# Kernel optimization log

Measured on AMD Instinct MI355X. Metric: run time of the kernel, lower is better.

Reference implementation:

```python
import jax, jax.numpy as jnp
import numpy as np
from jax import lax

BITWIDTH = 7
EPS = 1e-5


def ti_quant(x):
    """TiFloatToInt8: per-tensor int8 quantization with power-of-2 scale."""
    rng = jnp.max(jnp.abs(x))
    bw = jnp.ceil(jnp.log2(rng))
    exp = bw - BITWIDTH
    q = jnp.clip(jnp.round(x * 2.0 ** (BITWIDTH - bw)), -128.0, 127.0)
    return q, exp


def ti_conv(xv, xe, wv, we, pad):
    """TiConv2d: integer conv (simulated in f32, all values int-valued),
    int32 accumulate, then shift back to 8 bits; exponents add."""
    acc = lax.conv_general_dilated(
        xv, wv, window_strides=(1, 1), padding=[(pad, pad), (pad, pad)],
        dimension_numbers=("NCHW", "OIHW", "NCHW"))
    rng = jnp.max(jnp.abs(acc))
    bw = jnp.ceil(jnp.log2(rng))
    shift = jnp.maximum(bw - BITWIDTH, 0.0)
    q = jnp.clip(jnp.round(acc * 2.0 ** (-shift)), -128.0, 127.0)
    return q, xe + we + shift


def batchnorm(x, gamma, beta):
    # training-mode BN: batch statistics over (N, H, W)
    mean = jnp.mean(x, axis=(0, 2, 3), keepdims=True)
    var = jnp.var(x, axis=(0, 2, 3), keepdims=True)
    g = gamma[None, :, None, None]
    b = beta[None, :, None, None]
    return g * (x - mean) * lax.rsqrt(var + EPS) + b


def setup_inputs() -> dict:
    key = jax.random.key(0)
    k0, k1, k2, k3, k4 = jax.random.split(key, 5)
    B, Cin, Cout, H, W = 32, 128, 256, 56, 56
    x_val = jax.random.randint(k0, (B, Cin, H, W), -128, 128, dtype=jnp.int32)
    x_exp = jnp.zeros((), jnp.float32) - 7.0
    wDW = jnp.round(jnp.clip(jax.random.normal(k1, (Cin, Cin, 3, 3), jnp.float32) * 32.0, -128.0, 127.0))
    wDW_exp = jnp.zeros((), jnp.float32) - 9.0
    wPW = jnp.round(jnp.clip(jax.random.normal(k2, (Cout, Cin, 1, 1), jnp.float32) * 32.0, -128.0, 127.0))
    wPW_exp = jnp.zeros((), jnp.float32) - 9.0
    gamma1 = jnp.ones((Cin,), jnp.float32) + 0.1 * jax.random.normal(k3, (Cin,), jnp.float32)
    beta1 = jnp.zeros((Cin,), jnp.float32)
    gamma2 = jnp.ones((Cout,), jnp.float32) + 0.1 * jax.random.normal(k4, (Cout,), jnp.float32)
    beta2 = jnp.zeros((Cout,), jnp.float32)
    return {"x_val": x_val, "x_exp": x_exp, "wDW": wDW, "wDW_exp": wDW_exp,
            "wPW": wPW, "wPW_exp": wPW_exp, "gamma1": gamma1, "beta1": beta1,
            "gamma2": gamma2, "beta2": beta2}


def reference(x_val, x_exp, wDW, wDW_exp, wPW, wPW_exp, gamma1, beta1, gamma2, beta2):
    xv = x_val.astype(jnp.float32)
    # convDW (3x3, in->in, pad=1)
    q, e = ti_conv(xv, x_exp, wDW, wDW_exp, 1)
    # dequant -> bn1 -> quant
    f = batchnorm(q * 2.0 ** e, gamma1, beta1)
    q, e = ti_quant(f)
    # TiReLU on int values
    q = jnp.maximum(q, 0.0)
    # convPW (1x1, in->out)
    q, e = ti_conv(q, e, wPW, wPW_exp, 0)
    # dequant -> bn2 -> quant -> relu
    f = batchnorm(q * 2.0 ** e, gamma2, beta2)
    q, e = ti_quant(f)
    q = jnp.maximum(q, 0.0)
    return q.astype(jnp.int8), e
```

## Files before the change

kernel.cpp:

```cpp
#include <hip/hip_runtime.h>
#include <cstdint>
#include <cstddef>

#define C1 128
#define C2 256
#define Hh 56
#define Wd 56
#define HW 3136
#define NHW 100352
#define N1 ((size_t)12845056)
#define N2 ((size_t)25690112)
#define XPSZ ((size_t)13778944)

typedef int v4i __attribute__((ext_vector_type(4)));
typedef int v16i __attribute__((ext_vector_type(16)));

static constexpr size_t OFF_XP = 0;
static constexpr size_t OFF_ACC1 = XPSZ;
static constexpr size_t OFF_Q1 = OFF_ACC1 + 4 * N1;
static constexpr size_t OFF_Q3 = OFF_Q1 + N1;
static constexpr size_t OFF_WQ1 = OFF_Q3 + N2;
static constexpr size_t OFF_WQ2 = OFF_WQ1 + 147456;
static constexpr size_t OFF_STATS = OFF_WQ2 + 32768;

struct Stats {
  int absmax1, absmax2, pad0, pad1;
  float scale1, e1, s2, e2;
  float scaleq2, e3, sf, ef;
  int sum1[C1]; unsigned sumsq1[C1];
  int min1[C1], max1[C1];
  float A1[C1], B1c[C1];
  int sum2[C2]; unsigned sumsq2[C2];
  int min2[C2], max2[C2];
  float A2[C2], B2c[C2];
};

__global__ void k_init(Stats* st) {
  int t = threadIdx.x;
  if (t == 0) { st->absmax1 = 0; st->absmax2 = 0; }
  for (int c = t; c < C1; c += 256) {
    st->sum1[c] = 0; st->sumsq1[c] = 0; st->min1[c] = 127; st->max1[c] = -128;
  }
  for (int c = t; c < C2; c += 256) {
    st->sum2[c] = 0; st->sumsq2[c] = 0; st->min2[c] = 127; st->max2[c] = -128;
  }
}

__global__ __launch_bounds__(256) void k_prep_x2(
    const int* __restrict__ x, signed char* __restrict__ xp) {
  __shared__ signed char lds[56 * 132];
  int t = threadIdx.x;
  int hh = blockIdx.x;
  int n = blockIdx.y;
  int* xpw = (int*)(xp + ((size_t)n * 58 + hh) * 7424);
  if (hh == 0 || hh == 57) {
    for (int o = t; o < 1856; o += 256) xpw[o] = 0;
    return;
  }
  int h = hh - 1;
  const int* xb = x + (size_t)n * C1 * HW + h * 56;
  for (int idx = t; idx < 7168; idx += 256) {
    int c = idx / 56, w = idx - c * 56;
    lds[w * 132 + c] = (signed char)xb[(size_t)c * HW + w];
  }
  __syncthreads();
  for (int o = t; o < 1856; o += 256) {
    int kb = o / 232, r = o - kb * 232, ww = r >> 2, cw = r & 3;
    int val = (ww == 0 || ww == 57) ? 0
              : *(const int*)&lds[(ww - 1) * 132 + kb * 16 + cw * 4];
    xpw[o] = val;
  }
}

__global__ void k_prep_w1(const float* __restrict__ wDW, signed char* __restrict__ wq1t) {
  int idx = blockIdx.x * 256 + threadIdx.x;
  if (idx >= 128 * 1152) return;
  int co = idx / 1152, r = idx - co * 1152;
  int ci = r / 9, pos = r - ci * 9;
  int k = pos * 128 + ci;
  wq1t[(size_t)(k >> 4) * 2048 + co * 16 + (k & 15)] = (signed char)(int)wDW[idx];
}

__global__ void k_prep_w2(const float* __restrict__ wPW, signed char* __restrict__ wq2t) {
  int i = blockIdx.x * 256 + threadIdx.x;
  int co = i >> 7, ci = i & 127;
  wq2t[(size_t)(ci >> 4) * 4096 + co * 16 + (ci & 15)] = (signed char)(int)wPW[i];
}

__device__ inline v4i ld16_lds(const signed char* p) {
  const int2* q = (const int2*)p;
  int2 lo = q[0], hi = q[1];
  v4i r; r[0] = lo.x; r[1] = lo.y; r[2] = hi.x; r[3] = hi.y;
  return r;
}

__global__ __launch_bounds__(256, 2) void k_conv1s(
    const signed char* __restrict__ xp, const signed char* __restrict__ wq1t,
    int* __restrict__ acc1, Stats* st) {
  __shared__ int reda[4];
  int t = threadIdx.x, lane = t & 63, wave = t >> 6;
  int half = lane >> 5, l31 = lane & 31;
  size_t g0 = (size_t)blockIdx.x * 256;

  const signed char* ab[2];
#pragma unroll
  for (int i = 0; i < 2; ++i) {
    size_t gm = g0 + wave * 64 + i * 32 + l31;
    int n = (int)(gm / HW);
    int p = (int)(gm - (size_t)n * HW);
    int h = p / 56, w = p - h * 56;
    ab[i] = xp + ((size_t)n * 58 + h) * 7424 + w * 16 + half * 928;
  }
  const signed char* bb[4];
#pragma unroll
  for (int j = 0; j < 4; ++j)
    bb[j] = wq1t + (size_t)(j * 32 + l31) * 16 + half * 2048;

  v16i a1[2][4];
#pragma unroll
  for (int i = 0; i < 2; ++i)
#pragma unroll
    for (int j = 0; j < 4; ++j)
#pragma unroll
      for (int r = 0; r < 16; ++r) a1[i][j][r] = 0;

#pragma unroll
  for (int pos = 0; pos < 9; ++pos) {
    int kh = pos / 3, kw = pos - kh * 3;
    const signed char* a0p = ab[0] + kh * 7424 + kw * 16;
    const signed char* a1p = ab[1] + kh * 7424 + kw * 16;
#pragma unroll
    for (int kb = 0; kb < 8; kb += 2) {
      v4i af0 = *(const v4i*)(a0p + kb * 928);
      v4i af1 = *(const v4i*)(a1p + kb * 928);
      v4i bf[4];
#pragma unroll
      for (int j = 0; j < 4; ++j)
        bf[j] = *(const v4i*)(bb[j] + pos * 16384 + kb * 2048);
#pragma unroll
      for (int j = 0; j < 4; ++j) {
        a1[0][j] = __builtin_amdgcn_mfma_i32_32x32x32_i8(af0, bf[j], a1[0][j], 0, 0, 0);
        a1[1][j] = __builtin_amdgcn_mfma_i32_32x32x32_i8(af1, bf[j], a1[1][j], 0, 0, 0);
      }
    }
  }

  int am = 0;
#pragma unroll
  for (int i = 0; i < 2; ++i)
#pragma unroll
    for (int j = 0; j < 4; ++j)
#pragma unroll
      for (int r = 0; r < 16; ++r) am = max(am, abs(a1[i][j][r]));
  for (int off = 32; off; off >>= 1) am = max(am, __shfl_down(am, off, 64));
  if (lane == 0) reda[wave] = am;
  __syncthreads();
  if (t == 0)
    atomicMax(&st->absmax1, max(max(reda[0], reda[1]), max(reda[2], reda[3])));

  int* ob = acc1 + (size_t)blockIdx.x * 32768;
#pragma unroll
  for (int i = 0; i < 2; ++i)
#pragma unroll
    for (int j = 0; j < 4; ++j)
#pragma unroll
      for (int reg = 0; reg < 16; ++reg)
        ob[(((wave * 2 + i) * 4 + j) * 16 + reg) * 64 + lane] = a1[i][j][reg];
}

__global__ __launch_bounds__(256, 2) void k_qstats1(
    const int* __restrict__ acc1, signed char* __restrict__ q1, Stats* st,
    const float* __restrict__ x_exp, const float* __restrict__ wDW_exp) {
  __shared__ int qti[256 * 34];
  __shared__ int psum[C1], psq[C1], pmn[C1], pmx[C1];
  signed char* qt = (signed char*)qti;
  int t = threadIdx.x, lane = t & 63, wave = t >> 6;
  int half = lane >> 5, l31 = lane & 31;

  if (t < C1) { psum[t] = 0; psq[t] = 0; pmn[t] = 127; pmx[t] = -128; }
  __syncthreads();

  int v1 = st->absmax1;
  int pw = 31 - __clz(v1 | 1);
  int bw = ((v1 & (v1 - 1)) == 0) ? pw : pw + 1;
  int sh = max(bw - 7, 0);
  float scale1 = exp2f((float)(-sh));
  if (blockIdx.x == 0 && t == 0)
    st->e1 = x_exp[0] + wDW_exp[0] + (float)sh;

  const int* ib = acc1 + (size_t)blockIdx.x * 32768;
#pragma unroll
  for (int j = 0; j < 4; ++j) {
    int sj = 0, sqj = 0, mnj = 127, mxj = -128;
    int c = j * 32 + l31;
#pragma unroll
    for (int i = 0; i < 2; ++i)
#pragma unroll
      for (int reg = 0; reg < 16; ++reg) {
        int av = ib[(((wave * 2 + i) * 4 + j) * 16 + reg) * 64 + lane];
        int row = (reg & 3) + 8 * (reg >> 2) + 4 * half;
        int pix = wave * 64 + i * 32 + row;
        float r = rintf((float)av * scale1);
        r = fminf(fmaxf(r, -128.f), 127.f);
        int qi = (int)r;
        qt[pix * 136 + c] = (signed char)qi;
        sj += qi; sqj += qi * qi; mnj = min(mnj, qi); mxj = max(mxj, qi);
      }
    sj += __shfl_down(sj, 32, 64);
    sqj += __shfl_down(sqj, 32, 64);
    mnj = min(mnj, __shfl_down(mnj, 32, 64));
    mxj = max(mxj, __shfl_down(mxj, 32, 64));
    if (half == 0) {
      atomicAdd(&psum[c], sj); atomicAdd(&psq[c], sqj);
      atomicMin(&pmn[c], mnj); atomicMax(&pmx[c], mxj);
    }
  }
  __syncthreads();
  if (t < C1) {
    atomicAdd(&st->sum1[t], psum[t]);
    atomicAdd(&st->sumsq1[t], (unsigned)psq[t]);
    atomicMin(&st->min1[t], pmn[t]);
    atomicMax(&st->max1[t], pmx[t]);
  }
  int* q1w = (int*)(q1 + (size_t)blockIdx.x * 256 * 128);
  for (int idx = t; idx < 8192; idx += 256) {
    int pix = idx >> 5, c4 = idx & 31;
    q1w[idx] = qti[pix * 34 + c4];
  }
}

template <int STORE>
__global__ __launch_bounds__(256, 2) void k_conv2t(
    const signed char* __restrict__ q1, const signed char* __restrict__ wq2t,
    signed char* __restrict__ q3, Stats* st, const float* __restrict__ wPW_exp) {
  __shared__ int qti[128 * 34];
  __shared__ signed char stg[128 * 264];
  __shared__ int psum[C2], psq[C2], pmn[C2], pmx[C2];
  __shared__ int reda[4];
  signed char* qt = (signed char*)qti;

  int t = threadIdx.x, lane = t & 63, wave = t >> 6;
  int half = lane >> 5, l31 = lane & 31;
  size_t g0 = (size_t)blockIdx.x * 128;

  if (STORE) { psum[t] = 0; psq[t] = 0; pmn[t] = 127; pmx[t] = -128; }

  int c4 = t & 31;
  float Av[4], Bv[4];
#pragma unroll
  for (int jj = 0; jj < 4; ++jj) {
    Av[jj] = st->A1[c4 * 4 + jj];
    Bv[jj] = st->B1c[c4 * 4 + jj];
  }
  float s2 = st->s2;
  const int* q1w = (const int*)(q1 + g0 * 128);
#pragma unroll
  for (int k = 0; k < 16; ++k) {
    int idx = k * 256 + t;
    int v = q1w[idx];
    int pix = idx >> 5;
    int outv = 0;
#pragma unroll
    for (int jj = 0; jj < 4; ++jj) {
      int b = (signed char)(v >> (8 * jj));
      float y = Av[jj] * (float)b + Bv[jj];
      float r = rintf(y * s2);
      r = fminf(fmaxf(r, -128.f), 127.f);
      r = fmaxf(r, 0.f);
      outv |= ((int)r & 0xff) << (8 * jj);
    }
    qti[pix * 34 + c4] = outv;
  }
  __syncthreads();

  v16i acc[8];
#pragma unroll
  for (int j = 0; j < 8; ++j)
#pragma unroll
    for (int r = 0; r < 16; ++r) acc[j][r] = 0;

#pragma unroll
  for (int ks = 0; ks < 4; ++ks) {
    v4i af = ld16_lds(&qt[(wave * 32 + l31) * 136 + half * 16 + ks * 32]);
#pragma unroll
    for (int j = 0; j < 8; ++j) {
      v4i bf = *(const v4i*)(wq2t + (size_t)(ks * 2 + half) * 4096 + (j * 32 + l31) * 16);
      acc[j] = __builtin_amdgcn_mfma_i32_32x32x32_i8(af, bf, acc[j], 0, 0, 0);
    }
  }

  if (STORE == 0) {
    int am2 = 0;
#pragma unroll
    for (int j = 0; j < 8; ++j)
#pragma unroll
      for (int r = 0; r < 16; ++r) am2 = max(am2, abs(acc[j][r]));
    for (int off = 32; off; off >>= 1) am2 = max(am2, __shfl_down(am2, off, 64));
    if (lane == 0) reda[wave] = am2;
    __syncthreads();
    if (t == 0)
      atomicMax(&st->absmax2, max(max(reda[0], reda[1]), max(reda[2], reda[3])));
  } else {
    int v2 = st->absmax2;
    int pw = 31 - __clz(v2 | 1);
    int bw = ((v2 & (v2 - 1)) == 0) ? pw : pw + 1;
    int sh2 = max(bw - 7, 0);
    float scale2 = exp2f((float)(-sh2));
    if (blockIdx.x == 0 && t == 0)
      st->e3 = st->e2 + wPW_exp[0] + (float)sh2;
#pragma unroll
    for (int j = 0; j < 8; ++j) {
      int c = j * 32 + l31;
      int sj = 0, sqj = 0, mnj = 127, mxj = -128;
#pragma unroll
      for (int reg = 0; reg < 16; ++reg) {
        int row = (reg & 3) + 8 * (reg >> 2) + 4 * half;
        float r = rintf((float)acc[j][reg] * scale2);
        r = fminf(fmaxf(r, -128.f), 127.f);
        int qi = (int)r;
        stg[(wave * 32 + row) * 264 + c] = (signed char)qi;
        sj += qi; sqj += qi * qi; mnj = min(mnj, qi); mxj = max(mxj, qi);
      }
      sj += __shfl_down(sj, 32, 64);
      sqj += __shfl_down(sqj, 32, 64);
      mnj = min(mnj, __shfl_down(mnj, 32, 64));
      mxj = max(mxj, __shfl_down(mxj, 32, 64));
      if (half == 0) {
        atomicAdd(&psum[c], sj); atomicAdd(&psq[c], sqj);
        atomicMin(&pmn[c], mnj); atomicMax(&pmx[c], mxj);
      }
    }
    __syncthreads();
    atomicAdd(&st->sum2[t], psum[t]);
    atomicAdd(&st->sumsq2[t], (unsigned)psq[t]);
    atomicMin(&st->min2[t], pmn[t]);
    atomicMax(&st->max2[t], pmx[t]);
    int* q3w = (int*)(q3 + g0 * 256);
#pragma unroll
    for (int k = 0; k < 32; ++k) {
      int idx = k * 256 + t;
      int pix = idx >> 6, cw = idx & 63;
      q3w[idx] = *(const int*)&stg[pix * 264 + cw * 4];
    }
  }
}

__global__ void k_bn(const int* __restrict__ sums,
                     const unsigned* __restrict__ sumsqs,
                     const int* __restrict__ mins, const int* __restrict__ maxs,
                     const float* __restrict__ gamma, const float* __restrict__ beta,
                     const float* __restrict__ e_in,
                     float* A, float* Bc, float* s_out, float* e_out,
                     float* e_extra, int C) {
  __shared__ float red[4];
  int t = threadIdx.x;
  float e1 = *e_in;
  double meanq = (double)sums[t] / (double)NHW;
  double varq = (double)sumsqs[t] / (double)NHW - meanq * meanq;
  float se = exp2f(e1);
  float mean = (float)meanq * se;
  float var = (float)varq * se * se;
  float rsq = 1.0f / sqrtf(var + 1e-5f);
  float g = gamma[t], b = beta[t];
  float Avv = g * se * rsq;
  float Bvv = b - g * mean * rsq;
  A[t] = Avv; Bc[t] = Bvv;
  float cand = fmaxf(fabsf(Avv * (float)mins[t] + Bvv), fabsf(Avv * (float)maxs[t] + Bvv));
  for (int off = 32; off; off >>= 1) cand = fmaxf(cand, __shfl_down(cand, off, 64));
  int wave = t >> 6, lane = t & 63;
  if (lane == 0) red[wave] = cand;
  __syncthreads();
  if (t == 0) {
    float rng = red[0];
    for (int i = 1; i < C / 64; i++) rng = fmaxf(rng, red[i]);
    float bwv = ceilf(log2f(rng));
    *s_out = exp2f(7.0f - bwv);
    *e_out = bwv - 7.0f;
    if (e_extra) *e_extra = bwv - 7.0f;
  }
}

__global__ __launch_bounds__(256) void k_out(
    const signed char* __restrict__ q3, const Stats* __restrict__ st,
    float* __restrict__ out) {
  __shared__ signed char lds[64 * 260];
  int t = threadIdx.x, lane = t & 63, wave = t >> 6;
  size_t g0 = (size_t)blockIdx.x * 64;
  int n = (int)(g0 / HW), p0 = (int)(g0 - (size_t)n * HW);
  const int* q3w = (const int*)(q3 + g0 * 256);
#pragma unroll
  for (int k = 0; k < 16; ++k) {
    int idx = k * 256 + t;
    int pix = idx >> 6, cw = idx & 63;
    *(int*)&lds[pix * 260 + cw * 4] = q3w[idx];
  }
  __syncthreads();
  float sf = st->sf;
  float* ob = out + (size_t)n * C2 * HW + p0 + lane;
#pragma unroll
  for (int cg = 0; cg < 16; ++cg) {
    int v = *(const int*)&lds[lane * 260 + wave * 64 + cg * 4];
#pragma unroll
    for (int jj = 0; jj < 4; ++jj) {
      int c = wave * 64 + cg * 4 + jj;
      float y = st->A2[c] * (float)((signed char)(v >> (8 * jj))) + st->B2c[c];
      float r = rintf(y * sf);
      r = fminf(fmaxf(r, -128.f), 127.f);
      ob[(size_t)c * HW] = fmaxf(r, 0.f);
    }
  }
}

extern "C" void kernel_launch(void* const* d_in, const int* in_sizes, int n_in,
                              void* d_out, int out_size, void* d_ws, size_t ws_size,
                              hipStream_t stream) {
  const int* x = (const int*)d_in[0];
  const float* x_exp = (const float*)d_in[1];
  const float* wDW = (const float*)d_in[2];
  const float* wDW_exp = (const float*)d_in[3];
  const float* wPW = (const float*)d_in[4];
  const float* wPW_exp = (const float*)d_in[5];
  const float* gamma1 = (const float*)d_in[6];
  const float* beta1 = (const float*)d_in[7];
  const float* gamma2 = (const float*)d_in[8];
  const float* beta2 = (const float*)d_in[9];
  float* out = (float*)d_out;

  char* ws = (char*)d_ws;
  signed char* xp2 = (signed char*)(ws + OFF_XP);
  int* acc1 = (int*)(ws + OFF_ACC1);
  signed char* q1 = (signed char*)(ws + OFF_Q1);
  signed char* q3 = (signed char*)(ws + OFF_Q3);
  signed char* wq1t = (signed char*)(ws + OFF_WQ1);
  signed char* wq2t = (signed char*)(ws + OFF_WQ2);
  Stats* st = (Stats*)(ws + OFF_STATS);

  hipLaunchKernelGGL(k_init, dim3(1), dim3(256), 0, stream, st);
  hipLaunchKernelGGL(k_prep_x2, dim3(58, 32), dim3(256), 0, stream, x, xp2);
  hipLaunchKernelGGL(k_prep_w1, dim3(576), dim3(256), 0, stream, wDW, wq1t);
  hipLaunchKernelGGL(k_prep_w2, dim3(128), dim3(256), 0, stream, wPW, wq2t);

  hipLaunchKernelGGL(k_conv1s, dim3(392), dim3(256), 0, stream,
                     xp2, wq1t, acc1, st);
  hipLaunchKernelGGL(k_qstats1, dim3(392), dim3(256), 0, stream,
                     acc1, q1, st, x_exp, wDW_exp);
  hipLaunchKernelGGL(k_bn, dim3(1), dim3(C1), 0, stream,
                     st->sum1, st->sumsq1, st->min1, st->max1, gamma1, beta1,
                     &st->e1, st->A1, st->B1c, &st->s2, &st->e2, (float*)nullptr, C1);

  hipLaunchKernelGGL(k_conv2t<0>, dim3(784), dim3(256), 0, stream,
                     q1, wq2t, q3, st, wPW_exp);
  hipLaunchKernelGGL(k_conv2t<1>, dim3(784), dim3(256), 0, stream,
                     q1, wq2t, q3, st, wPW_exp);
  hipLaunchKernelGGL(k_bn, dim3(1), dim3(C2), 0, stream,
                     st->sum2, st->sumsq2, st->min2, st->max2, gamma2, beta2,
                     &st->e3, st->A2, st->B2c, &st->sf, &st->ef, out + N2, C2);
  hipLaunchKernelGGL(k_out, dim3(1568), dim3(256), 0, stream, q3, st, out);
}
```

Before: 295.8 us.

## Fuse conv1 with quant and BN1 via cooperative grid sync; recompute conv2 instead of storing q3

Merges the four prep kernels into one launch. Replaces the conv1 plus quant-stats plus BN1 chain with a single cooperative kernel that keeps accumulators in registers across grid syncs, so the int32 acc1 tensor never goes to memory. The q3 intermediate is dropped: a third conv2 pass recomputes the 1x1 conv and writes the final output directly, with BN2 coefficients computed per block. This trades extra MFMA work and redundant per-block BN math for less HBM traffic and fewer launches, and relies on all 392 blocks being co-resident, with a fallback path if the cooperative launch fails.

```diff
diff --git a/kernel.cpp b/kernel.cpp
--- a/kernel.cpp
+++ b/kernel.cpp
@@ -1,6 +1,9 @@
 #include <hip/hip_runtime.h>
+#include <hip/hip_cooperative_groups.h>
 #include <cstdint>
 #include <cstddef>
+
+namespace cg = cooperative_groups;
 
 #define C1 128
 #define C2 256
@@ -18,25 +21,63 @@
 static constexpr size_t OFF_XP = 0;
 static constexpr size_t OFF_ACC1 = XPSZ;
 static constexpr size_t OFF_Q1 = OFF_ACC1 + 4 * N1;
-static constexpr size_t OFF_Q3 = OFF_Q1 + N1;
-static constexpr size_t OFF_WQ1 = OFF_Q3 + N2;
+static constexpr size_t OFF_WQ1 = OFF_Q1 + N1;
 static constexpr size_t OFF_WQ2 = OFF_WQ1 + 147456;
 static constexpr size_t OFF_STATS = OFF_WQ2 + 32768;
 
 struct Stats {
   int absmax1, absmax2, pad0, pad1;
-  float scale1, e1, s2, e2;
-  float scaleq2, e3, sf, ef;
+  float e1, e2, e3, s2v;
+  float A1[C1], B1c[C1];
   int sum1[C1]; unsigned sumsq1[C1];
   int min1[C1], max1[C1];
-  float A1[C1], B1c[C1];
   int sum2[C2]; unsigned sumsq2[C2];
   int min2[C2], max2[C2];
-  float A2[C2], B2c[C2];
 };
 
-__global__ void k_init(Stats* st) {
-  int t = threadIdx.x;
+__global__ __launch_bounds__(256) void k_pre(
+    const int* __restrict__ x, signed char* __restrict__ xp,
+    const float* __restrict__ wDW, signed char* __restrict__ wq1t,
+    const float* __restrict__ wPW, signed char* __restrict__ wq2t,
+    Stats* st) {
+  __shared__ signed char lds[56 * 132];
+  int t = threadIdx.x, bid = blockIdx.x;
+  if (bid < 1856) {
+    int hh = bid % 58, n = bid / 58;
+    int* xpw = (int*)(xp + ((size_t)n * 58 + hh) * 7424);
+    if (hh == 0 || hh == 57) {
+      for (int o = t; o < 1856; o += 256) xpw[o] = 0;
+      return;
+    }
+    int h = hh - 1;
+    const int* xb = x + (size_t)n * C1 * HW + h * 56;
+    for (int idx = t; idx < 7168; idx += 256) {
+      int c = idx / 56, w = idx - c * 56;
+      lds[w * 132 + c] = (signed char)xb[(size_t)c * HW + w];
+    }
+    __syncthreads();
+    for (int o = t; o < 1856; o += 256) {
+      int kb = o / 232, r = o - kb * 232, ww = r >> 2, cw = r & 3;
+      int val = (ww == 0 || ww == 57) ? 0
+                : *(const int*)&lds[(ww - 1) * 132 + kb * 16 + cw * 4];
+      xpw[o] = val;
+    }
+    return;
+  }
+  if (bid < 2432) {
+    int idx = (bid - 1856) * 256 + t;
+    int co = idx / 1152, r = idx - co * 1152;
+    int ci = r / 9, pos = r - ci * 9;
+    int k = pos * 128 + ci;
+    wq1t[(size_t)(k >> 4) * 2048 + co * 16 + (k & 15)] = (signed char)(int)wDW[idx];
+    return;
+  }
+  if (bid < 2560) {
+    int i = (bid - 2432) * 256 + t;
+    int co = i >> 7, ci = i & 127;
+    wq2t[(size_t)(ci >> 4) * 4096 + co * 16 + (ci & 15)] = (signed char)(int)wPW[i];
+    return;
+  }
   if (t == 0) { st->absmax1 = 0; st->absmax2 = 0; }
   for (int c = t; c < C1; c += 256) {
     st->sum1[c] = 0; st->sumsq1[c] = 0; st->min1[c] = 127; st->max1[c] = -128;
@@ -44,47 +85,6 @@
   for (int c = t; c < C2; c += 256) {
     st->sum2[c] = 0; st->sumsq2[c] = 0; st->min2[c] = 127; st->max2[c] = -128;
   }
-}
-
-__global__ __launch_bounds__(256) void k_prep_x2(
-    const int* __restrict__ x, signed char* __restrict__ xp) {
-  __shared__ signed char lds[56 * 132];
-  int t = threadIdx.x;
-  int hh = blockIdx.x;
-  int n = blockIdx.y;
-  int* xpw = (int*)(xp + ((size_t)n * 58 + hh) * 7424);
-  if (hh == 0 || hh == 57) {
-    for (int o = t; o < 1856; o += 256) xpw[o] = 0;
-    return;
-  }
-  int h = hh - 1;
-  const int* xb = x + (size_t)n * C1 * HW + h * 56;
-  for (int idx = t; idx < 7168; idx += 256) {
-    int c = idx / 56, w = idx - c * 56;
-    lds[w * 132 + c] = (signed char)xb[(size_t)c * HW + w];
-  }
-  __syncthreads();
-  for (int o = t; o < 1856; o += 256) {
-    int kb = o / 232, r = o - kb * 232, ww = r >> 2, cw = r & 3;
-    int val = (ww == 0 || ww == 57) ? 0
-              : *(const int*)&lds[(ww - 1) * 132 + kb * 16 + cw * 4];
-    xpw[o] = val;
-  }
-}
-
-__global__ void k_prep_w1(const float* __restrict__ wDW, signed char* __restrict__ wq1t) {
-  int idx = blockIdx.x * 256 + threadIdx.x;
-  if (idx >= 128 * 1152) return;
-  int co = idx / 1152, r = idx - co * 1152;
-  int ci = r / 9, pos = r - ci * 9;
-  int k = pos * 128 + ci;
-  wq1t[(size_t)(k >> 4) * 2048 + co * 16 + (k & 15)] = (signed char)(int)wDW[idx];
-}
-
-__global__ void k_prep_w2(const float* __restrict__ wPW, signed char* __restrict__ wq2t) {
-  int i = blockIdx.x * 256 + threadIdx.x;
-  int co = i >> 7, ci = i & 127;
-  wq2t[(size_t)(ci >> 4) * 4096 + co * 16 + (ci & 15)] = (signed char)(int)wPW[i];
 }
 
 __device__ inline v4i ld16_lds(const signed char* p) {
@@ -92,6 +92,165 @@
   int2 lo = q[0], hi = q[1];
   v4i r; r[0] = lo.x; r[1] = lo.y; r[2] = hi.x; r[3] = hi.y;
   return r;
+}
+
+__device__ inline float bn_affine_v(int sum, unsigned sumsq, int mn, int mx,
+                                    float g, float b, float e_in,
+                                    float* Aout, float* Bout) {
+  double meanq = (double)sum / (double)NHW;
+  double varq = (double)sumsq / (double)NHW - meanq * meanq;
+  float se = exp2f(e_in);
+  float mean = (float)meanq * se;
+  float var = (float)varq * se * se;
+  float rsq = 1.0f / sqrtf(var + 1e-5f);
+  float Avv = g * se * rsq;
+  float Bvv = b - g * mean * rsq;
+  *Aout = Avv; *Bout = Bvv;
+  return fmaxf(fabsf(Avv * (float)mn + Bvv), fabsf(Avv * (float)mx + Bvv));
+}
+
+__global__ __launch_bounds__(256, 2) void k_conv1f(
+    const signed char* __restrict__ xp, const signed char* __restrict__ wq1t,
+    signed char* __restrict__ q1, Stats* st,
+    const float* __restrict__ x_exp, const float* __restrict__ wDW_exp,
+    const float* __restrict__ gamma1, const float* __restrict__ beta1) {
+  __shared__ int reda[4];
+  __shared__ int vbro;
+  __shared__ int qti[256 * 34];
+  __shared__ int psum[C1], psq[C1], pmn[C1], pmx[C1];
+  __shared__ float redc[2];
+  signed char* qt = (signed char*)qti;
+  int t = threadIdx.x, lane = t & 63, wave = t >> 6;
+  int half = lane >> 5, l31 = lane & 31;
+  size_t g0 = (size_t)blockIdx.x * 256;
+
+  const signed char* ab[2];
+#pragma unroll
+  for (int i = 0; i < 2; ++i) {
+    size_t gm = g0 + wave * 64 + i * 32 + l31;
+    int n = (int)(gm / HW);
+    int p = (int)(gm - (size_t)n * HW);
+    int h = p / 56, w = p - h * 56;
+    ab[i] = xp + ((size_t)n * 58 + h) * 7424 + w * 16 + half * 928;
+  }
+  const signed char* bb[4];
+#pragma unroll
+  for (int j = 0; j < 4; ++j)
+    bb[j] = wq1t + (size_t)(j * 32 + l31) * 16 + half * 2048;
+
+  v16i a1[2][4];
+#pragma unroll
+  for (int i = 0; i < 2; ++i)
+#pragma unroll
+    for (int j = 0; j < 4; ++j)
+#pragma unroll
+      for (int r = 0; r < 16; ++r) a1[i][j][r] = 0;
+
+#pragma unroll
+  for (int pos = 0; pos < 9; ++pos) {
+    int kh = pos / 3, kw = pos - kh * 3;
+    const signed char* a0p = ab[0] + kh * 7424 + kw * 16;
+    const signed char* a1p = ab[1] + kh * 7424 + kw * 16;
+#pragma unroll
+    for (int kb = 0; kb < 8; kb += 2) {
+      v4i af0 = *(const v4i*)(a0p + kb * 928);
+      v4i af1 = *(const v4i*)(a1p + kb * 928);
+      v4i bf[4];
+#pragma unroll
+      for (int j = 0; j < 4; ++j)
+        bf[j] = *(const v4i*)(bb[j] + pos * 16384 + kb * 2048);
+#pragma unroll
+      for (int j = 0; j < 4; ++j) {
+        a1[0][j] = __builtin_amdgcn_mfma_i32_32x32x32_i8(af0, bf[j], a1[0][j], 0, 0, 0);
+        a1[1][j] = __builtin_amdgcn_mfma_i32_32x32x32_i8(af1, bf[j], a1[1][j], 0, 0, 0);
+      }
+    }
+  }
+
+  int am = 0;
+#pragma unroll
+  for (int i = 0; i < 2; ++i)
+#pragma unroll
+    for (int j = 0; j < 4; ++j)
+#pragma unroll
+      for (int r = 0; r < 16; ++r) am = max(am, abs(a1[i][j][r]));
+  for (int off = 32; off; off >>= 1) am = max(am, __shfl_down(am, off, 64));
+  if (lane == 0) reda[wave] = am;
+  __syncthreads();
+  if (t == 0)
+    atomicMax(&st->absmax1, max(max(reda[0], reda[1]), max(reda[2], reda[3])));
+  if (t < C1) { psum[t] = 0; psq[t] = 0; pmn[t] = 127; pmx[t] = -128; }
+
+  cg::this_grid().sync();
+
+  if (t == 0) vbro = atomicMax(&st->absmax1, 0);
+  __syncthreads();
+  int v1 = vbro;
+  int pw = 31 - __clz(v1 | 1);
+  int bw = ((v1 & (v1 - 1)) == 0) ? pw : pw + 1;
+  int sh = max(bw - 7, 0);
+  float scale1 = exp2f((float)(-sh));
+  if (blockIdx.x == 0 && t == 0)
+    st->e1 = x_exp[0] + wDW_exp[0] + (float)sh;
+
+#pragma unroll
+  for (int j = 0; j < 4; ++j) {
+    int sj = 0, sqj = 0, mnj = 127, mxj = -128;
+    int c = j * 32 + l31;
+#pragma unroll
+    for (int i = 0; i < 2; ++i)
+#pragma unroll
+      for (int reg = 0; reg < 16; ++reg) {
+        int av = a1[i][j][reg];
+        int row = (reg & 3) + 8 * (reg >> 2) + 4 * half;
+        int pix = wave * 64 + i * 32 + row;
+        float r = rintf((float)av * scale1);
+        r = fminf(fmaxf(r, -128.f), 127.f);
+        int qi = (int)r;
+        qt[pix * 136 + c] = (signed char)qi;
+        sj += qi; sqj += qi * qi; mnj = min(mnj, qi); mxj = max(mxj, qi);
+      }
+    sj += __shfl_down(sj, 32, 64);
+    sqj += __shfl_down(sqj, 32, 64);
+    mnj = min(mnj, __shfl_down(mnj, 32, 64));
+    mxj = max(mxj, __shfl_down(mxj, 32, 64));
+    if (half == 0) {
+      atomicAdd(&psum[c], sj); atomicAdd(&psq[c], sqj);
+      atomicMin(&pmn[c], mnj); atomicMax(&pmx[c], mxj);
+    }
+  }
+  __syncthreads();
+  if (t < C1) {
+    atomicAdd(&st->sum1[t], psum[t]);
+    atomicAdd(&st->sumsq1[t], (unsigned)psq[t]);
+    atomicMin(&st->min1[t], pmn[t]);
+    atomicMax(&st->max1[t], pmx[t]);
+  }
+  int* q1w = (int*)(q1 + g0 * 128);
+  for (int idx = t; idx < 8192; idx += 256)
+    q1w[idx] = qti[(idx >> 5) * 34 + (idx & 31)];
+
+  cg::this_grid().sync();
+
+  if (blockIdx.x == 0) {
+    if (t < C1) {
+      int sm = atomicAdd(&st->sum1[t], 0);
+      unsigned sq = atomicAdd(&st->sumsq1[t], 0u);
+      int mn = atomicMin(&st->min1[t], 127);
+      int mx = atomicMax(&st->max1[t], -128);
+      float cand = bn_affine_v(sm, sq, mn, mx, gamma1[t], beta1[t], st->e1,
+                               &st->A1[t], &st->B1c[t]);
+      for (int off = 32; off; off >>= 1) cand = fmaxf(cand, __shfl_down(cand, off, 64));
+      if ((t & 63) == 0) redc[t >> 6] = cand;
+    }
+    __syncthreads();
+    if (t == 0) {
+      float rng = fmaxf(redc[0], redc[1]);
+      float bwv = ceilf(log2f(rng));
+      st->s2v = exp2f(7.0f - bwv);
+      st->e2 = bwv - 7.0f;
+    }
+  }
 }
 
 __global__ __launch_bounds__(256, 2) void k_conv1s(
@@ -223,18 +382,33 @@
     atomicMax(&st->max1[t], pmx[t]);
   }
   int* q1w = (int*)(q1 + (size_t)blockIdx.x * 256 * 128);
-  for (int idx = t; idx < 8192; idx += 256) {
-    int pix = idx >> 5, c4 = idx & 31;
-    q1w[idx] = qti[pix * 34 + c4];
-  }
-}
-
-template <int STORE>
-__global__ __launch_bounds__(256, 2) void k_conv2t(
+  for (int idx = t; idx < 8192; idx += 256)
+    q1w[idx] = qti[(idx >> 5) * 34 + (idx & 31)];
+}
+
+__global__ void k_bn1f(Stats* st, const float* __restrict__ gamma1,
+                       const float* __restrict__ beta1) {
+  __shared__ float red[2];
+  int t = threadIdx.x;
+  float cand = bn_affine_v(st->sum1[t], st->sumsq1[t], st->min1[t], st->max1[t],
+                           gamma1[t], beta1[t], st->e1, &st->A1[t], &st->B1c[t]);
+  for (int off = 32; off; off >>= 1) cand = fmaxf(cand, __shfl_down(cand, off, 64));
+  if ((t & 63) == 0) red[t >> 6] = cand;
+  __syncthreads();
+  if (t == 0) {
+    float rng = fmaxf(red[0], red[1]);
+    float bwv = ceilf(log2f(rng));
+    st->s2v = exp2f(7.0f - bwv);
+    st->e2 = bwv - 7.0f;
+  }
+}
+
+template <int PASS>
+__global__ __launch_bounds__(256, 2) void k_conv2(
     const signed char* __restrict__ q1, const signed char* __restrict__ wq2t,
-    signed char* __restrict__ q3, Stats* st, const float* __restrict__ wPW_exp) {
+    Stats* st, const float* __restrict__ wPW_exp) {
   __shared__ int qti[128 * 34];
-  __shared__ signed char stg[128 * 264];
+  __shared__ float A1l[C1], B1l[C1];
   __shared__ int psum[C2], psq[C2], pmn[C2], pmx[C2];
   __shared__ int reda[4];
   signed char* qt = (signed char*)qti;
@@ -243,16 +417,18 @@
   int half = lane >> 5, l31 = lane & 31;
   size_t g0 = (size_t)blockIdx.x * 128;
 
-  if (STORE) { psum[t] = 0; psq[t] = 0; pmn[t] = 127; pmx[t] = -128; }
+  if (t < C1) { A1l[t] = st->A1[t]; B1l[t] = st->B1c[t]; }
+  if (PASS) { psum[t] = 0; psq[t] = 0; pmn[t] = 127; pmx[t] = -128; }
+  __syncthreads();
+  float s2 = st->s2v;
 
   int c4 = t & 31;
   float Av[4], Bv[4];
 #pragma unroll
   for (int jj = 0; jj < 4; ++jj) {
-    Av[jj] = st->A1[c4 * 4 + jj];
-    Bv[jj] = st->B1c[c4 * 4 + jj];
-  }
-  float s2 = st->s2;
+    Av[jj] = A1l[c4 * 4 + jj];
+    Bv[jj] = B1l[c4 * 4 + jj];
+  }
   const int* q1w = (const int*)(q1 + g0 * 128);
 #pragma unroll
   for (int k = 0; k < 16; ++k) {
@@ -263,7 +439,7 @@
 #pragma unroll
     for (int jj = 0; jj < 4; ++jj) {
       int b = (signed char)(v >> (8 * jj));
-      float y = Av[jj] * (float)b + Bv[jj];
+      float y = __builtin_fmaf(Av[jj], (float)b, Bv[jj]);
       float r = rintf(y * s2);
       r = fminf(fmaxf(r, -128.f), 127.f);
       r = fmaxf(r, 0.f);
@@ -289,7 +465,7 @@
     }
   }
 
-  if (STORE == 0) {
+  if (PASS == 0) {
     int am2 = 0;
 #pragma unroll
     for (int j = 0; j < 8; ++j)
@@ -314,11 +490,9 @@
       int sj = 0, sqj = 0, mnj = 127, mxj = -128;
 #pragma unroll
       for (int reg = 0; reg < 16; ++reg) {
-        int row = (reg & 3) + 8 * (reg >> 2) + 4 * half;
         float r = rintf((float)acc[j][reg] * scale2);
         r = fminf(fmaxf(r, -128.f), 127.f);
         int qi = (int)r;
-        stg[(wave * 32 + row) * 264 + c] = (signed char)qi;
         sj += qi; sqj += qi * qi; mnj = min(mnj, qi); mxj = max(mxj, qi);
       }
       sj += __shfl_down(sj, 32, 64);
@@ -335,78 +509,117 @@
     atomicAdd(&st->sumsq2[t], (unsigned)psq[t]);
     atomicMin(&st->min2[t], pmn[t]);
     atomicMax(&st->max2[t], pmx[t]);
-    int* q3w = (int*)(q3 + g0 * 256);
-#pragma unroll
-    for (int k = 0; k < 32; ++k) {
-      int idx = k * 256 + t;
-      int pix = idx >> 6, cw = idx & 63;
-      q3w[idx] = *(const int*)&stg[pix * 264 + cw * 4];
-    }
-  }
-}
-
-__global__ void k_bn(const int* __restrict__ sums,
-                     const unsigned* __restrict__ sumsqs,
-                     const int* __restrict__ mins, const int* __restrict__ maxs,
-                     const float* __restrict__ gamma, const float* __restrict__ beta,
-                     const float* __restrict__ e_in,
-                     float* A, float* Bc, float* s_out, float* e_out,
-                     float* e_extra, int C) {
-  __shared__ float red[4];
-  int t = threadIdx.x;
-  float e1 = *e_in;
-  double meanq = (double)sums[t] / (double)NHW;
-  double varq = (double)sumsqs[t] / (double)NHW - meanq * meanq;
-  float se = exp2f(e1);
-  float mean = (float)meanq * se;
-  float var = (float)varq * se * se;
-  float rsq = 1.0f / sqrtf(var + 1e-5f);
-  float g = gamma[t], b = beta[t];
-  float Avv = g * se * rsq;
-  float Bvv = b - g * mean * rsq;
-  A[t] = Avv; Bc[t] = Bvv;
-  float cand = fmaxf(fabsf(Avv * (float)mins[t] + Bvv), fabsf(Avv * (float)maxs[t] + Bvv));
-  for (int off = 32; off; off >>= 1) cand = fmaxf(cand, __shfl_down(cand, off, 64));
-  int wave = t >> 6, lane = t & 63;
-  if (lane == 0) red[wave] = cand;
+  }
+}
+
+__global__ __launch_bounds__(256, 2) void k_out2(
+    const signed char* __restrict__ q1, const signed char* __restrict__ wq2t,
+    Stats* st, const float* __restrict__ gamma2, const float* __restrict__ beta2,
+    float* __restrict__ out) {
+  __shared__ int qti[128 * 34];
+  __shared__ __align__(16) signed char stg[128 * 264];
+  __shared__ float A1l[C1], B1l[C1], A2l[C2], B2l[C2];
+  __shared__ float red2[4], se2[2];
+  signed char* qt = (signed char*)qti;
+
+  int t = threadIdx.x, lane = t & 63, wave = t >> 6;
+  int half = lane >> 5, l31 = lane & 31;
+  size_t g0 = (size_t)blockIdx.x * 128;
+
+  if (t < C1) { A1l[t] = st->A1[t]; B1l[t] = st->B1c[t]; }
+  {
+    float cand = bn_affine_v(st->sum2[t], st->sumsq2[t], st->min2[t], st->max2[t],
+                             gamma2[t], beta2[t], st->e3, &A2l[t], &B2l[t]);
+    for (int off = 32; off; off >>= 1) cand = fmaxf(cand, __shfl_down(cand, off, 64));
+    if ((t & 63) == 0) red2[t >> 6] = cand;
+  }
   __syncthreads();
   if (t == 0) {
-    float rng = red[0];
-    for (int i = 1; i < C / 64; i++) rng = fmaxf(rng, red[i]);
+    float rng = fmaxf(fmaxf(red2[0], red2[1]), fmaxf(red2[2], red2[3]));
     float bwv = ceilf(log2f(rng));
-    *s_out = exp2f(7.0f - bwv);
-    *e_out = bwv - 7.0f;
-    if (e_extra) *e_extra = bwv - 7.0f;
-  }
-}
-
-__global__ __launch_bounds__(256) void k_out(
-    const signed char* __restrict__ q3, const Stats* __restrict__ st,
-    float* __restrict__ out) {
-  __shared__ signed char lds[64 * 260];
-  int t = threadIdx.x, lane = t & 63, wave = t >> 6;
-  size_t g0 = (size_t)blockIdx.x * 64;
-  int n = (int)(g0 / HW), p0 = (int)(g0 - (size_t)n * HW);
-  const int* q3w = (const int*)(q3 + g0 * 256);
+    se2[0] = exp2f(7.0f - bwv); se2[1] = bwv - 7.0f;
+  }
+  __syncthreads();
+  float s2 = st->s2v, sf = se2[0];
+  if (blockIdx.x == 0 && t == 0) out[N2] = se2[1];
+
+  int c4 = t & 31;
+  float Av[4], Bv[4];
+#pragma unroll
+  for (int jj = 0; jj < 4; ++jj) {
+    Av[jj] = A1l[c4 * 4 + jj];
+    Bv[jj] = B1l[c4 * 4 + jj];
+  }
+  const int* q1w = (const int*)(q1 + g0 * 128);
 #pragma unroll
   for (int k = 0; k < 16; ++k) {
     int idx = k * 256 + t;
-    int pix = idx >> 6, cw = idx & 63;
-    *(int*)&lds[pix * 260 + cw * 4] = q3w[idx];
-  }
-  __syncthreads();
-  float sf = st->sf;
-  float* ob = out + (size_t)n * C2 * HW + p0 + lane;
-#pragma unroll
-  for (int cg = 0; cg < 16; ++cg) {
-    int v = *(const int*)&lds[lane * 260 + wave * 64 + cg * 4];
+    int v = q1w[idx];
+    int pix = idx >> 5;
+    int outv = 0;
 #pragma unroll
     for (int jj = 0; jj < 4; ++jj) {
-      int c = wave * 64 + cg * 4 + jj;
-      float y = st->A2[c] * (float)((signed char)(v >> (8 * jj))) + st->B2c[c];
-      float r = rintf(y * sf);
+      int b = (signed char)(v >> (8 * jj));
+      float y = __builtin_fmaf(Av[jj], (float)b, Bv[jj]);
+      float r = rintf(y * s2);
       r = fminf(fmaxf(r, -128.f), 127.f);
-      ob[(size_t)c * HW] = fmaxf(r, 0.f);
+      r = fmaxf(r, 0.f);
+      outv |= ((int)r & 0xff) << (8 * jj);
+    }
+    qti[pix * 34 + c4] = outv;
+  }
+  __syncthreads();
+
+  v16i acc[8];
+#pragma unroll
+  for (int j = 0; j < 8; ++j)
+#pragma unroll
+    for (int r = 0; r < 16; ++r) acc[j][r] = 0;
+
+#pragma unroll
+  for (int ks = 0; ks < 4; ++ks) {
+    v4i af = ld16_lds(&qt[(wave * 32 + l31) * 136 + half * 16 + ks * 32]);
+#pragma unroll
+    for (int j = 0; j < 8; ++j) {
+      v4i bf = *(const v4i*)(wq2t + (size_t)(ks * 2 + half) * 4096 + (j * 32 + l31) * 16);
+      acc[j] = __builtin_amdgcn_mfma_i32_32x32x32_i8(af, bf, acc[j], 0, 0, 0);
+    }
+  }
+
+  int v2 = st->absmax2;
+  int pw = 31 - __clz(v2 | 1);
+  int bw = ((v2 & (v2 - 1)) == 0) ? pw : pw + 1;
+  int sh2 = max(bw - 7, 0);
+  float scale2 = exp2f((float)(-sh2));
+#pragma unroll
+  for (int j = 0; j < 8; ++j) {
+    int c = j * 32 + l31;
+#pragma unroll
+    for (int reg = 0; reg < 16; ++reg) {
+      int row = (reg & 3) + 8 * (reg >> 2) + 4 * half;
+      float r = rintf((float)acc[j][reg] * scale2);
+      r = fminf(fmaxf(r, -128.f), 127.f);
+      stg[(wave * 32 + row) * 264 + c] = (signed char)(int)r;
+    }
+  }
+  __syncthreads();
+
+#pragma unroll
+  for (int g = 0; g < 2; ++g) {
+    size_t p = g0 + (size_t)g * 64;
+    int n = (int)(p / HW), p0 = (int)(p - (size_t)n * HW);
+    float* ob = out + (size_t)n * C2 * HW + p0 + lane;
+#pragma unroll
+    for (int cg = 0; cg < 16; ++cg) {
+      int v = *(const int*)&stg[(g * 64 + lane) * 264 + wave * 64 + cg * 4];
+#pragma unroll
+      for (int jj = 0; jj < 4; ++jj) {
+        int c = wave * 64 + cg * 4 + jj;
+        float y = __builtin_fmaf(A2l[c], (float)((signed char)(v >> (8 * jj))), B2l[c]);
+        float r = rintf(y * sf);
+        r = fminf(fmaxf(r, -128.f), 127.f);
+        ob[(size_t)c * HW] = fmaxf(r, 0.f);
+      }
     }
   }
 }
@@ -430,30 +643,30 @@
   signed char* xp2 = (signed char*)(ws + OFF_XP);
   int* acc1 = (int*)(ws + OFF_ACC1);
   signed char* q1 = (signed char*)(ws + OFF_Q1);
-  signed char* q3 = (signed char*)(ws + OFF_Q3);
   signed char* wq1t = (signed char*)(ws + OFF_WQ1);
   signed char* wq2t = (signed char*)(ws + OFF_WQ2);
   Stats* st = (Stats*)(ws + OFF_STATS);
 
-  hipLaunchKernelGGL(k_init, dim3(1), dim3(256), 0, stream, st);
-  hipLaunchKernelGGL(k_prep_x2, dim3(58, 32), dim3(256), 0, stream, x, xp2);
-  hipLaunchKernelGGL(k_prep_w1, dim3(576), dim3(256), 0, stream, wDW, wq1t);
-  hipLaunchKernelGGL(k_prep_w2, dim3(128), dim3(256), 0, stream, wPW, wq2t);
-
-  hipLaunchKernelGGL(k_conv1s, dim3(392), dim3(256), 0, stream,
-                     xp2, wq1t, acc1, st);
-  hipLaunchKernelGGL(k_qstats1, dim3(392), dim3(256), 0, stream,
-                     acc1, q1, st, x_exp, wDW_exp);
-  hipLaunchKernelGGL(k_bn, dim3(1), dim3(C1), 0, stream,
-                     st->sum1, st->sumsq1, st->min1, st->max1, gamma1, beta1,
-                     &st->e1, st->A1, st->B1c, &st->s2, &st->e2, (float*)nullptr, C1);
-
-  hipLaunchKernelGGL(k_conv2t<0>, dim3(784), dim3(256), 0, stream,
-                     q1, wq2t, q3, st, wPW_exp);
-  hipLaunchKernelGGL(k_conv2t<1>, dim3(784), dim3(256), 0, stream,
-                     q1, wq2t, q3, st, wPW_exp);
-  hipLaunchKernelGGL(k_bn, dim3(1), dim3(C2), 0, stream,
-                     st->sum2, st->sumsq2, st->min2, st->max2, gamma2, beta2,
-                     &st->e3, st->A2, st->B2c, &st->sf, &st->ef, out + N2, C2);
-  hipLaunchKernelGGL(k_out, dim3(1568), dim3(256), 0, stream, q3, st, out);
-}
+  hipLaunchKernelGGL(k_pre, dim3(2561), dim3(256), 0, stream,
+                     x, xp2, wDW, wq1t, wPW, wq2t, st);
+
+  void* cargs[] = {(void*)&xp2, (void*)&wq1t, (void*)&q1, (void*)&st,
+                   (void*)&x_exp, (void*)&wDW_exp, (void*)&gamma1, (void*)&beta1};
+  hipError_t cerr = hipLaunchCooperativeKernel((void*)k_conv1f, dim3(392), dim3(256),
+                                               cargs, 0, stream);
+  if (cerr != hipSuccess) {
+    (void)hipGetLastError();
+    hipLaunchKernelGGL(k_conv1s, dim3(392), dim3(256), 0, stream,
+                       xp2, wq1t, acc1, st);
+    hipLaunchKernelGGL(k_qstats1, dim3(392), dim3(256), 0, stream,
+                       acc1, q1, st, x_exp, wDW_exp);
+    hipLaunchKernelGGL(k_bn1f, dim3(1), dim3(128), 0, stream, st, gamma1, beta1);
+  }
+
+  hipLaunchKernelGGL(HIP_KERNEL_NAME(k_conv2<0>), dim3(784), dim3(256), 0, stream,
+                     q1, wq2t, st, wPW_exp);
+  hipLaunchKernelGGL(HIP_KERNEL_NAME(k_conv2<1>), dim3(784), dim3(256), 0, stream,
+                     q1, wq2t, st, wPW_exp);
+  hipLaunchKernelGGL(k_out2, dim3(784), dim3(256), 0, stream,
+                     q1, wq2t, st, gamma2, beta2, out);
+}
```

Measured after the change: 419.7 us. 41.9% more time.

## Merge prep kernels and fold BN finalization into last-block epilogues

Applied to the files above, without the earlier changes.

Combines the init, input-pack and two weight-pack kernels into one launch with a block-index dispatch. It also removes the two single-block BN kernels by having the last finishing block of k_qstats1 and k_conv2t<1> (found through an atomic ticket counter plus threadfence) compute the BN affine coefficients and output scale. This cuts launch count and the serialized tiny-kernel gaps between stages. In exchange it adds atomics, fences and extra syncthreads to every block, and depends on the ticket counters being reset on each call.

```diff
diff --git a/kernel.cpp b/kernel.cpp
--- a/kernel.cpp
+++ b/kernel.cpp
@@ -24,7 +24,7 @@
 static constexpr size_t OFF_STATS = OFF_WQ2 + 32768;
 
 struct Stats {
-  int absmax1, absmax2, pad0, pad1;
+  int absmax1, absmax2, tick1, tick2;
   float scale1, e1, s2, e2;
   float scaleq2, e3, sf, ef;
   int sum1[C1]; unsigned sumsq1[C1];
@@ -35,56 +35,56 @@
   float A2[C2], B2c[C2];
 };
 
-__global__ void k_init(Stats* st) {
-  int t = threadIdx.x;
-  if (t == 0) { st->absmax1 = 0; st->absmax2 = 0; }
+__global__ __launch_bounds__(256) void k_pre(
+    const int* __restrict__ x, signed char* __restrict__ xp,
+    const float* __restrict__ wDW, signed char* __restrict__ wq1t,
+    const float* __restrict__ wPW, signed char* __restrict__ wq2t,
+    Stats* st) {
+  __shared__ signed char lds[56 * 132];
+  int t = threadIdx.x, bid = blockIdx.x;
+  if (bid < 1856) {
+    int hh = bid % 58, n = bid / 58;
+    int* xpw = (int*)(xp + ((size_t)n * 58 + hh) * 7424);
+    if (hh == 0 || hh == 57) {
+      for (int o = t; o < 1856; o += 256) xpw[o] = 0;
+      return;
+    }
+    int h = hh - 1;
+    const int* xb = x + (size_t)n * C1 * HW + h * 56;
+    for (int idx = t; idx < 7168; idx += 256) {
+      int c = idx / 56, w = idx - c * 56;
+      lds[w * 132 + c] = (signed char)xb[(size_t)c * HW + w];
+    }
+    __syncthreads();
+    for (int o = t; o < 1856; o += 256) {
+      int kb = o / 232, r = o - kb * 232, ww = r >> 2, cw = r & 3;
+      int val = (ww == 0 || ww == 57) ? 0
+                : *(const int*)&lds[(ww - 1) * 132 + kb * 16 + cw * 4];
+      xpw[o] = val;
+    }
+    return;
+  }
+  if (bid < 2432) {
+    int idx = (bid - 1856) * 256 + t;
+    int co = idx / 1152, r = idx - co * 1152;
+    int ci = r / 9, pos = r - ci * 9;
+    int k = pos * 128 + ci;
+    wq1t[(size_t)(k >> 4) * 2048 + co * 16 + (k & 15)] = (signed char)(int)wDW[idx];
+    return;
+  }
+  if (bid < 2560) {
+    int i = (bid - 2432) * 256 + t;
+    int co = i >> 7, ci = i & 127;
+    wq2t[(size_t)(ci >> 4) * 4096 + co * 16 + (ci & 15)] = (signed char)(int)wPW[i];
+    return;
+  }
+  if (t == 0) { st->absmax1 = 0; st->absmax2 = 0; st->tick1 = 0; st->tick2 = 0; }
   for (int c = t; c < C1; c += 256) {
     st->sum1[c] = 0; st->sumsq1[c] = 0; st->min1[c] = 127; st->max1[c] = -128;
   }
   for (int c = t; c < C2; c += 256) {
     st->sum2[c] = 0; st->sumsq2[c] = 0; st->min2[c] = 127; st->max2[c] = -128;
   }
-}
-
-__global__ __launch_bounds__(256) void k_prep_x2(
-    const int* __restrict__ x, signed char* __restrict__ xp) {
-  __shared__ signed char lds[56 * 132];
-  int t = threadIdx.x;
-  int hh = blockIdx.x;
-  int n = blockIdx.y;
-  int* xpw = (int*)(xp + ((size_t)n * 58 + hh) * 7424);
-  if (hh == 0 || hh == 57) {
-    for (int o = t; o < 1856; o += 256) xpw[o] = 0;
-    return;
-  }
-  int h = hh - 1;
-  const int* xb = x + (size_t)n * C1 * HW + h * 56;
-  for (int idx = t; idx < 7168; idx += 256) {
-    int c = idx / 56, w = idx - c * 56;
-    lds[w * 132 + c] = (signed char)xb[(size_t)c * HW + w];
-  }
-  __syncthreads();
-  for (int o = t; o < 1856; o += 256) {
-    int kb = o / 232, r = o - kb * 232, ww = r >> 2, cw = r & 3;
-    int val = (ww == 0 || ww == 57) ? 0
-              : *(const int*)&lds[(ww - 1) * 132 + kb * 16 + cw * 4];
-    xpw[o] = val;
-  }
-}
-
-__global__ void k_prep_w1(const float* __restrict__ wDW, signed char* __restrict__ wq1t) {
-  int idx = blockIdx.x * 256 + threadIdx.x;
-  if (idx >= 128 * 1152) return;
-  int co = idx / 1152, r = idx - co * 1152;
-  int ci = r / 9, pos = r - ci * 9;
-  int k = pos * 128 + ci;
-  wq1t[(size_t)(k >> 4) * 2048 + co * 16 + (k & 15)] = (signed char)(int)wDW[idx];
-}
-
-__global__ void k_prep_w2(const float* __restrict__ wPW, signed char* __restrict__ wq2t) {
-  int i = blockIdx.x * 256 + threadIdx.x;
-  int co = i >> 7, ci = i & 127;
-  wq2t[(size_t)(ci >> 4) * 4096 + co * 16 + (ci & 15)] = (signed char)(int)wPW[i];
 }
 
 __device__ inline v4i ld16_lds(const signed char* p) {
@@ -92,6 +92,21 @@
   int2 lo = q[0], hi = q[1];
   v4i r; r[0] = lo.x; r[1] = lo.y; r[2] = hi.x; r[3] = hi.y;
   return r;
+}
+
+__device__ inline float bn_affine_v(int sum, unsigned sumsq, int mn, int mx,
+                                    float g, float b, float e_in,
+                                    float* Aout, float* Bout) {
+  double meanq = (double)sum / (double)NHW;
+  double varq = (double)sumsq / (double)NHW - meanq * meanq;
+  float se = exp2f(e_in);
+  float mean = (float)meanq * se;
+  float var = (float)varq * se * se;
+  float rsq = 1.0f / sqrtf(var + 1e-5f);
+  float Avv = g * se * rsq;
+  float Bvv = b - g * mean * rsq;
+  *Aout = Avv; *Bout = Bvv;
+  return fmaxf(fabsf(Avv * (float)mn + Bvv), fabsf(Avv * (float)mx + Bvv));
 }
 
 __global__ __launch_bounds__(256, 2) void k_conv1s(
@@ -170,9 +185,12 @@
 
 __global__ __launch_bounds__(256, 2) void k_qstats1(
     const int* __restrict__ acc1, signed char* __restrict__ q1, Stats* st,
-    const float* __restrict__ x_exp, const float* __restrict__ wDW_exp) {
+    const float* __restrict__ x_exp, const float* __restrict__ wDW_exp,
+    const float* __restrict__ gamma1, const float* __restrict__ beta1) {
   __shared__ int qti[256 * 34];
   __shared__ int psum[C1], psq[C1], pmn[C1], pmx[C1];
+  __shared__ float redc[2];
+  __shared__ int lastf;
   signed char* qt = (signed char*)qti;
   int t = threadIdx.x, lane = t & 63, wave = t >> 6;
   int half = lane >> 5, l31 = lane & 31;
@@ -185,8 +203,8 @@
   int bw = ((v1 & (v1 - 1)) == 0) ? pw : pw + 1;
   int sh = max(bw - 7, 0);
   float scale1 = exp2f((float)(-sh));
-  if (blockIdx.x == 0 && t == 0)
-    st->e1 = x_exp[0] + wDW_exp[0] + (float)sh;
+  float e1 = x_exp[0] + wDW_exp[0] + (float)sh;
+  if (blockIdx.x == 0 && t == 0) st->e1 = e1;
 
   const int* ib = acc1 + (size_t)blockIdx.x * 32768;
 #pragma unroll
@@ -223,20 +241,46 @@
     atomicMax(&st->max1[t], pmx[t]);
   }
   int* q1w = (int*)(q1 + (size_t)blockIdx.x * 256 * 128);
-  for (int idx = t; idx < 8192; idx += 256) {
-    int pix = idx >> 5, c4 = idx & 31;
-    q1w[idx] = qti[pix * 34 + c4];
+  for (int idx = t; idx < 8192; idx += 256)
+    q1w[idx] = qti[(idx >> 5) * 34 + (idx & 31)];
+
+  __syncthreads();
+  __threadfence();
+  if (t == 0) lastf = (atomicAdd(&st->tick1, 1) == 391);
+  __syncthreads();
+  if (lastf) {
+    if (t < C1) {
+      int sm = atomicAdd(&st->sum1[t], 0);
+      unsigned sq = atomicAdd(&st->sumsq1[t], 0u);
+      int mn = atomicMin(&st->min1[t], 127);
+      int mx = atomicMax(&st->max1[t], -128);
+      float cand = bn_affine_v(sm, sq, mn, mx, gamma1[t], beta1[t], e1,
+                               &st->A1[t], &st->B1c[t]);
+      for (int off = 32; off; off >>= 1) cand = fmaxf(cand, __shfl_down(cand, off, 64));
+      if ((t & 63) == 0) redc[t >> 6] = cand;
+    }
+    __syncthreads();
+    if (t == 0) {
+      float rng = fmaxf(redc[0], redc[1]);
+      float bwv = ceilf(log2f(rng));
+      st->s2 = exp2f(7.0f - bwv);
+      st->e2 = bwv - 7.0f;
+    }
   }
 }
 
 template <int STORE>
 __global__ __launch_bounds__(256, 2) void k_conv2t(
     const signed char* __restrict__ q1, const signed char* __restrict__ wq2t,
-    signed char* __restrict__ q3, Stats* st, const float* __restrict__ wPW_exp) {
+    signed char* __restrict__ q3, Stats* st, const float* __restrict__ wPW_exp,
+    const float* __restrict__ gamma2, const float* __restrict__ beta2,
+    float* __restrict__ out) {
   __shared__ int qti[128 * 34];
   __shared__ signed char stg[128 * 264];
   __shared__ int psum[C2], psq[C2], pmn[C2], pmx[C2];
   __shared__ int reda[4];
+  __shared__ float red2[4];
+  __shared__ int lastf;
   signed char* qt = (signed char*)qti;
 
   int t = threadIdx.x, lane = t & 63, wave = t >> 6;
@@ -306,8 +350,8 @@
     int bw = ((v2 & (v2 - 1)) == 0) ? pw : pw + 1;
     int sh2 = max(bw - 7, 0);
     float scale2 = exp2f((float)(-sh2));
-    if (blockIdx.x == 0 && t == 0)
-      st->e3 = st->e2 + wPW_exp[0] + (float)sh2;
+    float e3 = st->e2 + wPW_exp[0] + (float)sh2;
+    if (blockIdx.x == 0 && t == 0) st->e3 = e3;
 #pragma unroll
     for (int j = 0; j < 8; ++j) {
       int c = j * 32 + l31;
@@ -342,41 +386,29 @@
       int pix = idx >> 6, cw = idx & 63;
       q3w[idx] = *(const int*)&stg[pix * 264 + cw * 4];
     }
-  }
-}
-
-__global__ void k_bn(const int* __restrict__ sums,
-                     const unsigned* __restrict__ sumsqs,
-                     const int* __restrict__ mins, const int* __restrict__ maxs,
-                     const float* __restrict__ gamma, const float* __restrict__ beta,
-                     const float* __restrict__ e_in,
-                     float* A, float* Bc, float* s_out, float* e_out,
-                     float* e_extra, int C) {
-  __shared__ float red[4];
-  int t = threadIdx.x;
-  float e1 = *e_in;
-  double meanq = (double)sums[t] / (double)NHW;
-  double varq = (double)sumsqs[t] / (double)NHW - meanq * meanq;
-  float se = exp2f(e1);
-  float mean = (float)meanq * se;
-  float var = (float)varq * se * se;
-  float rsq = 1.0f / sqrtf(var + 1e-5f);
-  float g = gamma[t], b = beta[t];
-  float Avv = g * se * rsq;
-  float Bvv = b - g * mean * rsq;
-  A[t] = Avv; Bc[t] = Bvv;
-  float cand = fmaxf(fabsf(Avv * (float)mins[t] + Bvv), fabsf(Avv * (float)maxs[t] + Bvv));
-  for (int off = 32; off; off >>= 1) cand = fmaxf(cand, __shfl_down(cand, off, 64));
-  int wave = t >> 6, lane = t & 63;
-  if (lane == 0) red[wave] = cand;
-  __syncthreads();
-  if (t == 0) {
-    float rng = red[0];
-    for (int i = 1; i < C / 64; i++) rng = fmaxf(rng, red[i]);
-    float bwv = ceilf(log2f(rng));
-    *s_out = exp2f(7.0f - bwv);
-    *e_out = bwv - 7.0f;
-    if (e_extra) *e_extra = bwv - 7.0f;
+
+    __syncthreads();
+    __threadfence();
+    if (t == 0) lastf = (atomicAdd(&st->tick2, 1) == 783);
+    __syncthreads();
+    if (lastf) {
+      int sm = atomicAdd(&st->sum2[t], 0);
+      unsigned sq = atomicAdd(&st->sumsq2[t], 0u);
+      int mn = atomicMin(&st->min2[t], 127);
+      int mx = atomicMax(&st->max2[t], -128);
+      float cand = bn_affine_v(sm, sq, mn, mx, gamma2[t], beta2[t], e3,
+                               &st->A2[t], &st->B2c[t]);
+      for (int off = 32; off; off >>= 1) cand = fmaxf(cand, __shfl_down(cand, off, 64));
+      if (lane == 0) red2[wave] = cand;
+      __syncthreads();
+      if (t == 0) {
+        float rng = fmaxf(fmaxf(red2[0], red2[1]), fmaxf(red2[2], red2[3]));
+        float bwv = ceilf(log2f(rng));
+        st->sf = exp2f(7.0f - bwv);
+        st->ef = bwv - 7.0f;
+        out[N2] = bwv - 7.0f;
+      }
+    }
   }
 }
 
@@ -435,25 +467,15 @@
   signed char* wq2t = (signed char*)(ws + OFF_WQ2);
   Stats* st = (Stats*)(ws + OFF_STATS);
 
-  hipLaunchKernelGGL(k_init, dim3(1), dim3(256), 0, stream, st);
-  hipLaunchKernelGGL(k_prep_x2, dim3(58, 32), dim3(256), 0, stream, x, xp2);
-  hipLaunchKernelGGL(k_prep_w1, dim3(576), dim3(256), 0, stream, wDW, wq1t);
-  hipLaunchKernelGGL(k_prep_w2, dim3(128), dim3(256), 0, stream, wPW, wq2t);
-
+  hipLaunchKernelGGL(k_pre, dim3(2561), dim3(256), 0, stream,
+                     x, xp2, wDW, wq1t, wPW, wq2t, st);
   hipLaunchKernelGGL(k_conv1s, dim3(392), dim3(256), 0, stream,
                      xp2, wq1t, acc1, st);
   hipLaunchKernelGGL(k_qstats1, dim3(392), dim3(256), 0, stream,
-                     acc1, q1, st, x_exp, wDW_exp);
-  hipLaunchKernelGGL(k_bn, dim3(1), dim3(C1), 0, stream,
-                     st->sum1, st->sumsq1, st->min1, st->max1, gamma1, beta1,
-                     &st->e1, st->A1, st->B1c, &st->s2, &st->e2, (float*)nullptr, C1);
-
-  hipLaunchKernelGGL(k_conv2t<0>, dim3(784), dim3(256), 0, stream,
-                     q1, wq2t, q3, st, wPW_exp);
-  hipLaunchKernelGGL(k_conv2t<1>, dim3(784), dim3(256), 0, stream,
-                     q1, wq2t, q3, st, wPW_exp);
-  hipLaunchKernelGGL(k_bn, dim3(1), dim3(C2), 0, stream,
-                     st->sum2, st->sumsq2, st->min2, st->max2, gamma2, beta2,
-                     &st->e3, st->A2, st->B2c, &st->sf, &st->ef, out + N2, C2);
+                     acc1, q1, st, x_exp, wDW_exp, gamma1, beta1);
+  hipLaunchKernelGGL(HIP_KERNEL_NAME(k_conv2t<0>), dim3(784), dim3(256), 0, stream,
+                     q1, wq2t, q3, st, wPW_exp, gamma2, beta2, out);
+  hipLaunchKernelGGL(HIP_KERNEL_NAME(k_conv2t<1>), dim3(784), dim3(256), 0, stream,
+                     q1, wq2t, q3, st, wPW_exp, gamma2, beta2, out);
   hipLaunchKernelGGL(k_out, dim3(1568), dim3(256), 0, stream, q3, st, out);
 }
```

Result: slower. 392.0 us (+32.5%).
